# Performance work log

Hardware: AMD Instinct MI355X
Metric: run time of the kernel (lower is better)

## Reference

```python
import jax, jax.numpy as jnp
import numpy as np

OUT_FEATURES = 4096
IN_FEATURES = 4096
K = 4096
BLOCK_SIZE = 8
NUM_BLOCKS = OUT_FEATURES * IN_FEATURES // BLOCK_SIZE  # 2,097,152
ORIGINAL_NUMEL = OUT_FEATURES * IN_FEATURES


def setup_inputs() -> dict:
    key = jax.random.key(0)
    k1, k2, k3, k4 = jax.random.split(key, 4)
    x = jax.random.normal(k1, (4, 2048, IN_FEATURES), dtype=jnp.float32)
    codebook = jax.random.normal(k2, (K, BLOCK_SIZE), dtype=jnp.float32)
    indices = jax.random.randint(k3, (NUM_BLOCKS,), 0, K, dtype=jnp.int64)
    bias = jax.random.normal(k4, (OUT_FEATURES,), dtype=jnp.float32)
    return {"x": x, "codebook": codebook, "indices": indices, "bias": bias}


def reference(x, codebook, indices, bias):
    # Reconstruct weight from codebook: gather blocks, flatten, slice, reshape.
    reconstructed = codebook[indices]                      # [num_blocks, block_size]
    W = reconstructed.reshape(-1)[:ORIGINAL_NUMEL]
    W = W.reshape(OUT_FEATURES, IN_FEATURES)               # [out, in]
    # F.linear: x @ W^T + bias
    return jnp.einsum('bsi,oi->bso', x, W) + bias
```

## Files before the change

### kernel.cpp

```cpp
#include <hip/hip_runtime.h>
#include <stdint.h>


#define M_DIM 8192
#define N_DIM 4096
#define K_DIM 4096
#define BM 256
#define BN 256
#define BK 64
#define NT (K_DIM / BK)
#define NUM_W_BLOCKS 2097152

#define PW_WGS 2048
#define PX_WGS 4096
#define PX_OUT (M_DIM * K_DIM / 8)
#define PX_ITERS (PX_OUT / (PX_WGS * 256))

typedef __attribute__((ext_vector_type(8))) __bf16 bf16x8;
typedef __attribute__((ext_vector_type(4))) float floatx4;

__device__ __forceinline__ unsigned int f2bf(float f) {
    unsigned int u = __builtin_bit_cast(unsigned int, f);
    u += 0x7fffu + ((u >> 16) & 1u);
    return u >> 16;
}

__global__ __launch_bounds__(256) void prep_kernel(
    const float* __restrict__ cb, const int* __restrict__ idx,
    uint4* __restrict__ W, const float4* __restrict__ x4,
    uint4* __restrict__ xb4) {
    const int wg = blockIdx.x;
    const int tid = threadIdx.x;
    if (wg < PW_WGS) {
#pragma unroll
        for (int k = 0; k < 4; ++k) {
            const int b = (wg * 4 + k) * 256 + tid;
            const int id = idx[b];
            const float4* s = (const float4*)(cb + ((size_t)id << 3));
            const float4 a = s[0];
            const float4 c = s[1];
            uint4 o;
            o.x = f2bf(a.x) | (f2bf(a.y) << 16);
            o.y = f2bf(a.z) | (f2bf(a.w) << 16);
            o.z = f2bf(c.x) | (f2bf(c.y) << 16);
            o.w = f2bf(c.z) | (f2bf(c.w) << 16);
            W[b] = o;
        }
    } else {
        const int xwg = wg - PW_WGS;
#pragma unroll
        for (int it = 0; it < PX_ITERS; ++it) {
            const size_t o = ((size_t)(it * PX_WGS + xwg)) * 256 + tid;
            const float4 a = x4[2 * o];
            const float4 c = x4[2 * o + 1];
            uint4 v;
            v.x = f2bf(a.x) | (f2bf(a.y) << 16);
            v.y = f2bf(a.z) | (f2bf(a.w) << 16);
            v.z = f2bf(c.x) | (f2bf(c.y) << 16);
            v.w = f2bf(c.z) | (f2bf(c.w) << 16);
            xb4[o] = v;
        }
    }
}

__device__ __forceinline__ void async_copy16(const __bf16* g, __bf16* s) {
    __builtin_amdgcn_global_load_lds(
        (const __attribute__((address_space(1))) unsigned int*)(uintptr_t)g,
        (__attribute__((address_space(3))) unsigned int*)(uintptr_t)s,
        16, 0, 0);
}

#define STAGE(gsrc, arr, slotElems)                                        \
    do {                                                                   \
        async_copy16((gsrc), (arr) + (slotElems) + wave512);               \
        async_copy16((gsrc) + (size_t)128 * K_DIM,                         \
                     (arr) + (slotElems) + 4096 + wave512);                \
    } while (0)

__global__ __launch_bounds__(512, 2) void gemm_bt_kernel(
    const __bf16* __restrict__ A,
    const __bf16* __restrict__ B,
    const float* __restrict__ bias,
    float* __restrict__ C) {
    __shared__ __align__(16) __bf16 sA[4 * 8192];
    __shared__ __align__(16) __bf16 sB[4 * 8192];

    const int tid = threadIdx.x;
    const int wave = tid >> 6;
    const int lane = tid & 63;
    const int wr = wave >> 2;
    const int wc = wave & 3;

    const int flat = blockIdx.x;
    const int xcd = flat & 7;
    const int q = flat >> 3;
    const int half = q >> 5;
    const int sq = q & 31;
    const int m0 = ((xcd & 3) * 8 + half * 4 + (sq & 3)) * BM;
    const int n0 = ((xcd >> 2) * 8 + (sq >> 2)) * BN;

    const int srow = tid >> 2;
    const int schunk = ((tid & 3) ^ ((srow >> 1) & 3)) << 3;
    const __bf16* gA = A + (size_t)(m0 + srow) * K_DIM + schunk;
    const __bf16* gB = B + (size_t)(n0 + srow) * K_DIM + schunk;
    const int wave512 = wave << 9;

    const int fr = lane & 15;
    const int roff = fr * 32 + (((lane >> 4) ^ ((fr >> 1) & 3)) << 3);
    const int aBase = wr * 4096 + roff;
    const int bBase = wc * 2048 + roff;

    floatx4 acc[8][4] = {};

    STAGE(gA, sA, 0);
    STAGE(gB, sB, 0);
    STAGE(gA + 32, sA, 8192);
    STAGE(gB + 32, sB, 8192);
    STAGE(gA + 64, sA, 16384);
    STAGE(gB + 64, sB, 16384);
    asm volatile("s_waitcnt vmcnt(8)" ::: "memory");
    __builtin_amdgcn_s_barrier();

    for (int t = 0; t < NT; ++t) {
        const int cs = (t & 1) ? 16384 : 0;
        const int ns = cs ^ 16384;
        const __bf16* sA0 = sA + cs;
        const __bf16* sA1 = sA + cs + 8192;
        const __bf16* sB0 = sB + cs;
        const __bf16* sB1 = sB + cs + 8192;

        bf16x8 af0[4], af1[4], bfr[4];

#pragma unroll
        for (int i = 0; i < 4; ++i)
            af0[i] = *(const bf16x8*)(sA0 + aBase + i * 512);
#pragma unroll
        for (int j = 0; j < 4; ++j)
            bfr[j] = *(const bf16x8*)(sB0 + bBase + j * 512);
#pragma unroll
        for (int i = 0; i < 4; ++i)
            af1[i] = *(const bf16x8*)(sA0 + aBase + 2048 + i * 512);
        if (t + 1 < NT) {
            STAGE(gA + (size_t)(t + 1) * 64 + 32, sA, ns + 8192);
            STAGE(gB + (size_t)(t + 1) * 64 + 32, sB, ns + 8192);
        }
        __builtin_amdgcn_s_barrier();
        asm volatile("s_waitcnt lgkmcnt(0)" ::: "memory");
        __builtin_amdgcn_s_setprio(1);
#pragma unroll
        for (int i = 0; i < 4; ++i)
#pragma unroll
            for (int j = 0; j < 4; ++j)
                acc[i][j] = __builtin_amdgcn_mfma_f32_16x16x32_bf16(
                    af0[i], bfr[j], acc[i][j], 0, 0, 0);
#pragma unroll
        for (int i = 0; i < 4; ++i)
#pragma unroll
            for (int j = 0; j < 4; ++j)
                acc[i + 4][j] = __builtin_amdgcn_mfma_f32_16x16x32_bf16(
                    af1[i], bfr[j], acc[i + 4][j], 0, 0, 0);
        __builtin_amdgcn_s_setprio(0);
        if (t + 1 < NT)
            asm volatile("s_waitcnt vmcnt(8)" ::: "memory");
        else
            asm volatile("s_waitcnt vmcnt(0)" ::: "memory");
        __builtin_amdgcn_s_barrier();

#pragma unroll
        for (int i = 0; i < 4; ++i)
            af0[i] = *(const bf16x8*)(sA1 + aBase + i * 512);
#pragma unroll
        for (int j = 0; j < 4; ++j)
            bfr[j] = *(const bf16x8*)(sB1 + bBase + j * 512);
#pragma unroll
        for (int i = 0; i < 4; ++i)
            af1[i] = *(const bf16x8*)(sA1 + aBase + 2048 + i * 512);
        if (t + 2 < NT) {
            STAGE(gA + (size_t)(t + 2) * 64, sA, cs);
            STAGE(gB + (size_t)(t + 2) * 64, sB, cs);
        }
        __builtin_amdgcn_s_barrier();
        asm volatile("s_waitcnt lgkmcnt(0)" ::: "memory");
        __builtin_amdgcn_s_setprio(1);
#pragma unroll
        for (int i = 0; i < 4; ++i)
#pragma unroll
            for (int j = 0; j < 4; ++j)
                acc[i][j] = __builtin_amdgcn_mfma_f32_16x16x32_bf16(
                    af0[i], bfr[j], acc[i][j], 0, 0, 0);
#pragma unroll
        for (int i = 0; i < 4; ++i)
#pragma unroll
            for (int j = 0; j < 4; ++j)
                acc[i + 4][j] = __builtin_amdgcn_mfma_f32_16x16x32_bf16(
                    af1[i], bfr[j], acc[i + 4][j], 0, 0, 0);
        __builtin_amdgcn_s_setprio(0);
        if (t + 2 < NT)
            asm volatile("s_waitcnt vmcnt(8)" ::: "memory");
        else if (t + 1 < NT)
            asm volatile("s_waitcnt vmcnt(4)" ::: "memory");
        else
            asm volatile("s_waitcnt vmcnt(0)" ::: "memory");
        __builtin_amdgcn_s_barrier();
    }

    const int crow = (lane >> 4) * 4;
    const int ccol = lane & 15;
#pragma unroll
    for (int j = 0; j < 4; ++j) {
        const int n = n0 + wc * 64 + j * 16 + ccol;
        const float bv = bias[n];
#pragma unroll
        for (int i = 0; i < 8; ++i) {
            const int m = m0 + wr * 128 + i * 16 + crow;
            float* cp = C + (size_t)m * N_DIM + n;
#pragma unroll
            for (int r = 0; r < 4; ++r)
                __builtin_nontemporal_store(acc[i][j][r] + bv,
                                            cp + (size_t)r * N_DIM);
        }
    }
}

extern "C" void kernel_launch(void* const* d_in, const int* in_sizes, int n_in,
                              void* d_out, int out_size, void* d_ws, size_t ws_size,
                              hipStream_t stream) {
    const float* x    = (const float*)d_in[0];
    const float* cb   = (const float*)d_in[1];
    const int*   idx  = (const int*)d_in[2];
    const float* bias = (const float*)d_in[3];
    float* out = (float*)d_out;

    __bf16* Wb = (__bf16*)d_ws;
    __bf16* Xb = (__bf16*)((char*)d_ws + (size_t)N_DIM * K_DIM * sizeof(__bf16));

    prep_kernel<<<PW_WGS + PX_WGS, 256, 0, stream>>>(
        cb, idx, (uint4*)Wb, (const float4*)x, (uint4*)Xb);

    dim3 grid(M_DIM / BM * (N_DIM / BN));
    gemm_bt_kernel<<<grid, 512, 0, stream>>>(Xb, Wb, bias, out);
}
```

Measured before the change: 477.3 us.

## Simplify prep kernel to one element per thread and drop mid-iteration GEMM barrier

The prep kernel now launches one workgroup per 256 codebook blocks and one thread per 4 x floats. It uses nontemporal loads instead of unrolled multi-iteration loops. In the GEMM main loop, the async global-to-LDS copies are issued before the LDS fragment reads, and the extra s_barrier plus explicit lgkmcnt(0) wait between reads and MFMAs are removed. The goals are less barrier stall time and more memory parallelism in prep, at the cost of many more small workgroups and relying on the compiler to insert the LDS waits.

```diff
diff --git a/kernel.cpp b/kernel.cpp
--- a/kernel.cpp
+++ b/kernel.cpp
@@ -10,14 +10,12 @@
 #define BK 64
 #define NT (K_DIM / BK)
 #define NUM_W_BLOCKS 2097152
-
-#define PW_WGS 2048
-#define PX_WGS 4096
-#define PX_OUT (M_DIM * K_DIM / 8)
-#define PX_ITERS (PX_OUT / (PX_WGS * 256))
+#define W_WGS (NUM_W_BLOCKS / 256)
+#define X_WGS ((M_DIM * K_DIM / 4) / 256)
 
 typedef __attribute__((ext_vector_type(8))) __bf16 bf16x8;
 typedef __attribute__((ext_vector_type(4))) float floatx4;
+typedef __attribute__((ext_vector_type(2))) unsigned int uintx2;
 
 __device__ __forceinline__ unsigned int f2bf(float f) {
     unsigned int u = __builtin_bit_cast(unsigned int, f);
@@ -27,39 +25,28 @@
 
 __global__ __launch_bounds__(256) void prep_kernel(
     const float* __restrict__ cb, const int* __restrict__ idx,
-    uint4* __restrict__ W, const float4* __restrict__ x4,
-    uint4* __restrict__ xb4) {
+    uint4* __restrict__ W, const floatx4* __restrict__ x,
+    uintx2* __restrict__ xb) {
     const int wg = blockIdx.x;
-    const int tid = threadIdx.x;
-    if (wg < PW_WGS) {
-#pragma unroll
-        for (int k = 0; k < 4; ++k) {
-            const int b = (wg * 4 + k) * 256 + tid;
-            const int id = idx[b];
-            const float4* s = (const float4*)(cb + ((size_t)id << 3));
-            const float4 a = s[0];
-            const float4 c = s[1];
-            uint4 o;
-            o.x = f2bf(a.x) | (f2bf(a.y) << 16);
-            o.y = f2bf(a.z) | (f2bf(a.w) << 16);
-            o.z = f2bf(c.x) | (f2bf(c.y) << 16);
-            o.w = f2bf(c.z) | (f2bf(c.w) << 16);
-            W[b] = o;
-        }
+    if (wg < W_WGS) {
+        const int b = wg * 256 + threadIdx.x;
+        const int id = __builtin_nontemporal_load(idx + b);
+        const float4* s = (const float4*)(cb + ((size_t)id << 3));
+        const float4 a = s[0];
+        const float4 c = s[1];
+        uint4 o;
+        o.x = f2bf(a.x) | (f2bf(a.y) << 16);
+        o.y = f2bf(a.z) | (f2bf(a.w) << 16);
+        o.z = f2bf(c.x) | (f2bf(c.y) << 16);
+        o.w = f2bf(c.z) | (f2bf(c.w) << 16);
+        W[b] = o;
     } else {
-        const int xwg = wg - PW_WGS;
-#pragma unroll
-        for (int it = 0; it < PX_ITERS; ++it) {
-            const size_t o = ((size_t)(it * PX_WGS + xwg)) * 256 + tid;
-            const float4 a = x4[2 * o];
-            const float4 c = x4[2 * o + 1];
-            uint4 v;
-            v.x = f2bf(a.x) | (f2bf(a.y) << 16);
-            v.y = f2bf(a.z) | (f2bf(a.w) << 16);
-            v.z = f2bf(c.x) | (f2bf(c.y) << 16);
-            v.w = f2bf(c.z) | (f2bf(c.w) << 16);
-            xb4[o] = v;
-        }
+        const size_t t = (size_t)(wg - W_WGS) * 256 + threadIdx.x;
+        const floatx4 a = __builtin_nontemporal_load(x + t);
+        uintx2 o;
+        o.x = f2bf(a.x) | (f2bf(a.y) << 16);
+        o.y = f2bf(a.z) | (f2bf(a.w) << 16);
+        xb[t] = o;
     }
 }
 
@@ -131,21 +118,19 @@
 
         bf16x8 af0[4], af1[4], bfr[4];
 
-#pragma unroll
-        for (int i = 0; i < 4; ++i)
-            af0[i] = *(const bf16x8*)(sA0 + aBase + i * 512);
-#pragma unroll
-        for (int j = 0; j < 4; ++j)
-            bfr[j] = *(const bf16x8*)(sB0 + bBase + j * 512);
-#pragma unroll
-        for (int i = 0; i < 4; ++i)
-            af1[i] = *(const bf16x8*)(sA0 + aBase + 2048 + i * 512);
         if (t + 1 < NT) {
             STAGE(gA + (size_t)(t + 1) * 64 + 32, sA, ns + 8192);
             STAGE(gB + (size_t)(t + 1) * 64 + 32, sB, ns + 8192);
         }
-        __builtin_amdgcn_s_barrier();
-        asm volatile("s_waitcnt lgkmcnt(0)" ::: "memory");
+#pragma unroll
+        for (int i = 0; i < 4; ++i)
+            af0[i] = *(const bf16x8*)(sA0 + aBase + i * 512);
+#pragma unroll
+        for (int j = 0; j < 4; ++j)
+            bfr[j] = *(const bf16x8*)(sB0 + bBase + j * 512);
+#pragma unroll
+        for (int i = 0; i < 4; ++i)
+            af1[i] = *(const bf16x8*)(sA0 + aBase + 2048 + i * 512);
         __builtin_amdgcn_s_setprio(1);
 #pragma unroll
         for (int i = 0; i < 4; ++i)
@@ -166,21 +151,19 @@
             asm volatile("s_waitcnt vmcnt(0)" ::: "memory");
         __builtin_amdgcn_s_barrier();
 
-#pragma unroll
-        for (int i = 0; i < 4; ++i)
-            af0[i] = *(const bf16x8*)(sA1 + aBase + i * 512);
-#pragma unroll
-        for (int j = 0; j < 4; ++j)
-            bfr[j] = *(const bf16x8*)(sB1 + bBase + j * 512);
-#pragma unroll
-        for (int i = 0; i < 4; ++i)
-            af1[i] = *(const bf16x8*)(sA1 + aBase + 2048 + i * 512);
         if (t + 2 < NT) {
             STAGE(gA + (size_t)(t + 2) * 64, sA, cs);
             STAGE(gB + (size_t)(t + 2) * 64, sB, cs);
         }
-        __builtin_amdgcn_s_barrier();
-        asm volatile("s_waitcnt lgkmcnt(0)" ::: "memory");
+#pragma unroll
+        for (int i = 0; i < 4; ++i)
+            af0[i] = *(const bf16x8*)(sA1 + aBase + i * 512);
+#pragma unroll
+        for (int j = 0; j < 4; ++j)
+            bfr[j] = *(const bf16x8*)(sB1 + bBase + j * 512);
+#pragma unroll
+        for (int i = 0; i < 4; ++i)
+            af1[i] = *(const bf16x8*)(sA1 + aBase + 2048 + i * 512);
         __builtin_amdgcn_s_setprio(1);
 #pragma unroll
         for (int i = 0; i < 4; ++i)
@@ -234,8 +217,8 @@
     __bf16* Wb = (__bf16*)d_ws;
     __bf16* Xb = (__bf16*)((char*)d_ws + (size_t)N_DIM * K_DIM * sizeof(__bf16));
 
-    prep_kernel<<<PW_WGS + PX_WGS, 256, 0, stream>>>(
-        cb, idx, (uint4*)Wb, (const float4*)x, (uint4*)Xb);
+    prep_kernel<<<W_WGS + X_WGS, 256, 0, stream>>>(
+        cb, idx, (uint4*)Wb, (const floatx4*)x, (uintx2*)Xb);
 
     dim3 grid(M_DIM / BM * (N_DIM / BN));
     gemm_bt_kernel<<<grid, 512, 0, stream>>>(Xb, Wb, bias, out);
```

After: 460.5 us. 1.04x faster.
